# Optimization experiments

Measured on AMD Instinct MI355X. Metric: run time of the kernel, lower is better.

## Reference

```python
import jax, jax.numpy as jnp
import numpy as np
from functools import partial

BS, NQ, NC, NG = 16, 1000, 80, 200
EPS = 0.1
ITERS = 100
ALPHA, GAMMA = 0.25, 2.0
CC, CB, CG, CBG = 2.0, 5.0, 2.0, 1.0  # cost_class, cost_bbox, cost_giou, cost_bg
K, T_ITERS, T_CUR = 4, 6, 6


def setup_inputs() -> dict:
    key = jax.random.key(0)
    k0, k1, k2, k3 = jax.random.split(key, 4)
    pred_logits = jax.random.normal(k0, (BS, NQ, NC), jnp.float32)
    u = jax.random.uniform(k1, (BS, NQ, 4), jnp.float32)
    # valid xyxy boxes in image coordinates
    pred_boxes = jnp.concatenate([u[..., :2] * 1000.0,
                                  u[..., :2] * 1000.0 + u[..., 2:] * 200.0 + 1.0], axis=-1)
    gt_classes = jax.random.randint(k2, (BS, NG), 0, NC)
    v = jax.random.uniform(k3, (BS, NG, 4), jnp.float32)
    gt_boxes = jnp.concatenate([v[..., :2] * 1000.0,
                                v[..., :2] * 1000.0 + v[..., 2:] * 200.0 + 1.0], axis=-1)
    image_size_xyxy = jnp.tile(jnp.array([1333.0, 800.0, 1333.0, 800.0], jnp.float32), (BS, 1))
    image_size_xyxy_tgt = jnp.tile(image_size_xyxy[:, None, :], (1, NG, 1))
    return {"pred_logits": pred_logits, "pred_boxes": pred_boxes,
            "gt_classes": gt_classes, "gt_boxes": gt_boxes,
            "image_size_xyxy": image_size_xyxy, "image_size_xyxy_tgt": image_size_xyxy_tgt}


def pairwise_giou(a, b):
    # a: [G,4] xyxy, b: [Q,4] xyxy -> [G,Q]
    area_a = (a[:, 2] - a[:, 0]) * (a[:, 3] - a[:, 1])
    area_b = (b[:, 2] - b[:, 0]) * (b[:, 3] - b[:, 1])
    lt = jnp.maximum(a[:, None, :2], b[None, :, :2])
    rb = jnp.minimum(a[:, None, 2:], b[None, :, 2:])
    wh = jnp.clip(rb - lt, 0.0)
    inter = wh[..., 0] * wh[..., 1]
    union = area_a[:, None] + area_b[None, :] - inter
    iou = inter / union
    lt_c = jnp.minimum(a[:, None, :2], b[None, :, :2])
    rb_c = jnp.maximum(a[:, None, 2:], b[None, :, 2:])
    wh_c = jnp.clip(rb_c - lt_c, 0.0)
    area_c = wh_c[..., 0] * wh_c[..., 1]
    return iou - (area_c - union) / area_c


def sinkhorn_logdomain(mu, nu, C):
    # log-domain Sinkhorn, faithful to the torch loop (v update uses M^T)
    log_mu = jnp.log(mu + 1e-8)
    log_nu = jnp.log(nu + 1e-8)
    M = lambda u, v: (-C + u[:, None] + v[None, :]) / EPS

    def step(carry, _):
        u, v = carry
        v = EPS * (log_nu - jax.nn.logsumexp(M(u, v), axis=0)) + v
        u = EPS * (log_mu - jax.nn.logsumexp(M(u, v), axis=1)) + u
        return (u, v), None

    (u, v), _ = jax.lax.scan(step, (jnp.ones_like(mu), jnp.ones_like(nu)), None, length=ITERS)
    return jnp.exp(M(u, v))


def _per_image(logits, boxes, tgt_ids, tgt_bbox, img, img_tgt):
    # focal-loss classification cost without materializing [G,Q,C]:
    # for one-hot targets, loss_cls[g,q] = sum_c neg[q,c] + pos[q,id_g] - neg[q,id_g]
    p = jax.nn.sigmoid(logits)                                  # [Q,C]
    pos = ALPHA * jax.nn.softplus(-logits) * (1.0 - p) ** GAMMA  # target=1 term
    neg = (1.0 - ALPHA) * jax.nn.softplus(logits) * p ** GAMMA   # target=0 term
    neg_sum = neg.sum(axis=-1)                                   # [Q]
    delta = (pos - neg)[:, tgt_ids]                              # [Q,G]
    loss_cls = neg_sum[None, :] + delta.T                        # [G,Q]
    loss_bg = neg_sum                                            # [Q]

    out_b = boxes / img[None, :]
    tgt_b = tgt_bbox / img_tgt
    cost_bbox = jnp.abs(tgt_b[:, None, :] - out_b[None, :, :]).sum(-1)  # L1 cdist [G,Q]
    cost_giou = -pairwise_giou(tgt_bbox, boxes)                          # [G,Q]

    loss = CC * loss_cls + CB * cost_bbox + CG * cost_giou
    loss = jnp.concatenate([loss, CBG * loss_bg[None, :]], axis=0)       # [G+1,Q]

    # mu construction, faithful to original (scalar broadcast onto mu[:-1])
    fg = float(K) - 0.5 * (T_ITERS - T_CUR)
    mu_fg = float(NQ) - fg * NG
    mu = jnp.concatenate([jnp.full((NG,), mu_fg, loss.dtype), jnp.ones((1,), loss.dtype)])
    nu = jnp.ones((NQ,), loss.dtype)

    pi = sinkhorn_logdomain(mu, nu, loss)
    pi = pi / pi.max(axis=1, keepdims=True)
    matched_gt_inds = jnp.argmax(pi, axis=0)  # [Q], value NG means background
    return pi, matched_gt_inds


def reference(pred_logits, pred_boxes, gt_classes, gt_boxes, image_size_xyxy, image_size_xyxy_tgt):
    return jax.vmap(_per_image)(pred_logits, pred_boxes, gt_classes, gt_boxes,
                                image_size_xyxy, image_size_xyxy_tgt)
```

## Files before the change

kernel.cpp:

```cpp
#include <hip/hip_runtime.h>
#include <math.h>

#define NIMG 16
#define NQI  1000
#define NCC  80
#define NGG  200
#define RR   201
#define NR   208
#define RPT  13
#define NWG  16
#define CPW  63
#define NTHR 1024
#define NITER 100
#define LDW  68

#define LOG2E  1.4426950408889634f
#define SC     14.426950408889634f
#define U2INIT 14.426950408889634f
#define NEG    -1e30f

union MS { unsigned long long u; float2 f; };

__device__ __forceinline__ void img_barrier(unsigned* c, unsigned target) {
    __syncthreads();
    if (threadIdx.x == 0) {
        __hip_atomic_fetch_add(c, 1u, __ATOMIC_RELAXED, __HIP_MEMORY_SCOPE_AGENT);
        int spins = 0;
        while (__hip_atomic_load(c, __ATOMIC_RELAXED, __HIP_MEMORY_SCOPE_AGENT) < target) {
            if (++spins > (1 << 22)) break;
        }
    }
    __syncthreads();
}

extern "C" __global__ void __launch_bounds__(NTHR, 1)
ota_kernel(const float* __restrict__ logits,
           const float* __restrict__ pboxes,
           const int*   __restrict__ gcls,
           const float* __restrict__ gboxes,
           const float* __restrict__ imsz,
           const float* __restrict__ imszt,
           float* __restrict__ out,
           unsigned* __restrict__ cnt,
           unsigned long long* __restrict__ pms,
           float* __restrict__ pmx)
{
    const int tid = threadIdx.x;
    const int bid = blockIdx.x;
    const int img = (bid & 7) * 2 + ((bid >> 3) >> 4);
    const int wg  = (bid >> 3) & 15;
    const int q0  = wg * CPW;
    const int ncols = min(CPW, NQI - q0);
    unsigned* myc = cnt + img * 16;

    __shared__ __align__(16) float sA[NR * LDW];
    __shared__ float sU[NR];
    __shared__ float sRM[NR];

    float4* sTB4 = (float4*)sA;
    float4* sGB4 = (float4*)(sA + 800);
    float*  sGA  = sA + 1600;
    int*    sCL  = (int*)(sA + 1800);

    const float LMU2 = log2f(200.0f);

    for (int g = tid; g < NGG; g += NTHR) {
        float4 gb = *(const float4*)(gboxes + ((size_t)img * NGG + g) * 4);
        float4 t4 = *(const float4*)(imszt  + ((size_t)img * NGG + g) * 4);
        sGB4[g] = gb;
        sTB4[g] = make_float4(gb.x / t4.x, gb.y / t4.y, gb.z / t4.z, gb.w / t4.w);
        sGA[g] = (gb.z - gb.x) * (gb.w - gb.y);
        sCL[g] = gcls[(size_t)img * NGG + g];
    }
    if (tid < NR) sU[tid] = (tid < RR) ? U2INIT : NEG;
    __syncthreads();

    const int col  = tid >> 4;
    const int part = tid & 15;
    const int q    = q0 + col;
    const int r0   = part * RPT;

    const float* lp = logits + ((size_t)img * NQI + q) * NCC;

    float ns = 0.f;
    if (col < ncols) {
        for (int c = part; c < NCC; c += 16) {
            float l = lp[c];
            float p = 1.f / (1.f + exp2f(-l * LOG2E));
            float spl = fmaxf(l, 0.f) + log1pf(expf(-fabsf(l)));
            ns += 0.75f * spl * p * p;
        }
    }
    #pragma unroll
    for (int k = 1; k < 16; k <<= 1) ns += __shfl_xor(ns, k);

    float e[RPT];
    {
        float4 isz = *(const float4*)(imsz + img * 4);
        float4 pp = make_float4(0.f, 0.f, 0.f, 0.f);
        float ab = 0.f, ob0 = 0.f, ob1 = 0.f, ob2 = 0.f, ob3 = 0.f;
        if (col < ncols) {
            pp = *(const float4*)(pboxes + ((size_t)img * NQI + q) * 4);
            ab  = (pp.z - pp.x) * (pp.w - pp.y);
            ob0 = pp.x / isz.x; ob1 = pp.y / isz.y; ob2 = pp.z / isz.z; ob3 = pp.w / isz.w;
        }
        #pragma unroll
        for (int i = 0; i < RPT; ++i) {
            int g = r0 + i;
            float val = NEG;
            if (col < ncols) {
                if (g < NGG) {
                    float l = lp[sCL[g]];
                    float p = 1.f / (1.f + exp2f(-l * LOG2E));
                    float t0 = log1pf(expf(-fabsf(l)));
                    float spl  = fmaxf(l, 0.f) + t0;
                    float spml = spl - l;
                    float pos = 0.25f * spml * (1.f - p) * (1.f - p);
                    float neg = 0.75f * spl * p * p;
                    float lcls = ns + (pos - neg);
                    float4 tb = sTB4[g];
                    float cb = fabsf(tb.x - ob0) + fabsf(tb.y - ob1)
                             + fabsf(tb.z - ob2) + fabsf(tb.w - ob3);
                    float4 gb = sGB4[g];
                    float iwd = fminf(gb.z, pp.z) - fmaxf(gb.x, pp.x);
                    float ihd = fminf(gb.w, pp.w) - fmaxf(gb.y, pp.y);
                    float inter = fmaxf(iwd, 0.f) * fmaxf(ihd, 0.f);
                    float uni = sGA[g] + ab - inter;
                    float iou = inter / uni;
                    float cwd = fmaxf(gb.z, pp.z) - fminf(gb.x, pp.x);
                    float chd = fmaxf(gb.w, pp.w) - fminf(gb.y, pp.y);
                    float ac = fmaxf(cwd, 0.f) * fmaxf(chd, 0.f);
                    float giou = iou - (ac - uni) / ac;
                    float loss = 2.f * lcls + 5.f * cb - 2.f * giou;
                    val = -loss * SC;
                } else if (g == NGG) {
                    val = -ns * SC;
                }
            }
            e[i] = val;
        }
    }
    __syncthreads();

    const int r2 = tid >> 2, h = tid & 3;
    float vv = NEG;

    for (int it = 0; it < NITER; ++it) {
        {
            float M = NEG;
            float xr[RPT];
            #pragma unroll
            for (int i = 0; i < RPT; ++i) {
                float x = e[i] + sU[r0 + i];
                xr[i] = x; M = fmaxf(M, x);
            }
            #pragma unroll
            for (int k = 1; k < 16; k <<= 1) M = fmaxf(M, __shfl_xor(M, k));
            float S = 0.f;
            #pragma unroll
            for (int i = 0; i < RPT; ++i) S += exp2f(xr[i] - M);
            #pragma unroll
            for (int k = 1; k < 16; k <<= 1) S += __shfl_xor(S, k);
            vv = -(M + log2f(S));
            if (col >= ncols) vv = NEG;
        }
        #pragma unroll
        for (int i = 0; i < RPT; ++i) sA[(r0 + i) * LDW + col] = e[i] + vv;
        __syncthreads();
        unsigned long long* pb = pms + ((size_t)(it & 1) * NIMG + img) * (RR * NWG);
        if (r2 < RR) {
            const float4* base = (const float4*)(sA + r2 * LDW + h * 16);
            float4 t0 = base[0], t1 = base[1], t2 = base[2], t3 = base[3];
            float M2 = fmaxf(
                fmaxf(fmaxf(fmaxf(t0.x, t0.y), fmaxf(t0.z, t0.w)),
                      fmaxf(fmaxf(t1.x, t1.y), fmaxf(t1.z, t1.w))),
                fmaxf(fmaxf(fmaxf(t2.x, t2.y), fmaxf(t2.z, t2.w)),
                      fmaxf(fmaxf(t3.x, t3.y), fmaxf(t3.z, t3.w))));
            #pragma unroll
            for (int k = 1; k < 4; k <<= 1) M2 = fmaxf(M2, __shfl_xor(M2, k));
            float S2 = exp2f(t0.x - M2) + exp2f(t0.y - M2) + exp2f(t0.z - M2) + exp2f(t0.w - M2)
                     + exp2f(t1.x - M2) + exp2f(t1.y - M2) + exp2f(t1.z - M2) + exp2f(t1.w - M2)
                     + exp2f(t2.x - M2) + exp2f(t2.y - M2) + exp2f(t2.z - M2) + exp2f(t2.w - M2)
                     + exp2f(t3.x - M2) + exp2f(t3.y - M2) + exp2f(t3.z - M2) + exp2f(t3.w - M2);
            #pragma unroll
            for (int k = 1; k < 4; k <<= 1) S2 += __shfl_xor(S2, k);
            if (h == 0) {
                MS ms; ms.f.x = M2; ms.f.y = S2;
                __hip_atomic_store(&pb[r2 * NWG + wg], ms.u,
                                   __ATOMIC_RELAXED, __HIP_MEMORY_SCOPE_AGENT);
            }
        }
        img_barrier(myc, (unsigned)NWG * (it + 1));
        if (r2 < NR) {
            if (r2 < RR) {
                unsigned long long* pr = pb + r2 * NWG + h * 4;
                MS a0, a1, a2, a3;
                a0.u = __hip_atomic_load(&pr[0], __ATOMIC_RELAXED, __HIP_MEMORY_SCOPE_AGENT);
                a1.u = __hip_atomic_load(&pr[1], __ATOMIC_RELAXED, __HIP_MEMORY_SCOPE_AGENT);
                a2.u = __hip_atomic_load(&pr[2], __ATOMIC_RELAXED, __HIP_MEMORY_SCOPE_AGENT);
                a3.u = __hip_atomic_load(&pr[3], __ATOMIC_RELAXED, __HIP_MEMORY_SCOPE_AGENT);
                float gm = fmaxf(fmaxf(a0.f.x, a1.f.x), fmaxf(a2.f.x, a3.f.x));
                #pragma unroll
                for (int k = 1; k < 4; k <<= 1) gm = fmaxf(gm, __shfl_xor(gm, k));
                float S = a0.f.y * exp2f(a0.f.x - gm) + a1.f.y * exp2f(a1.f.x - gm)
                        + a2.f.y * exp2f(a2.f.x - gm) + a3.f.y * exp2f(a3.f.x - gm);
                #pragma unroll
                for (int k = 1; k < 4; k <<= 1) S += __shfl_xor(S, k);
                if (h == 0) sU[r2] = (r2 < NGG ? LMU2 : 0.f) - (gm + log2f(S));
            } else if (h == 0) {
                sU[r2] = NEG;
            }
        }
        __syncthreads();
    }

    float u2[RPT];
    #pragma unroll
    for (int i = 0; i < RPT; ++i) u2[i] = sU[r0 + i];
    #pragma unroll
    for (int i = 0; i < RPT; ++i) sA[(r0 + i) * LDW + col] = e[i] + u2[i] + vv;
    __syncthreads();
    if (r2 < RR) {
        const float4* base = (const float4*)(sA + r2 * LDW + h * 16);
        float4 t0 = base[0], t1 = base[1], t2 = base[2], t3 = base[3];
        float M2 = fmaxf(
            fmaxf(fmaxf(fmaxf(t0.x, t0.y), fmaxf(t0.z, t0.w)),
                  fmaxf(fmaxf(t1.x, t1.y), fmaxf(t1.z, t1.w))),
            fmaxf(fmaxf(fmaxf(t2.x, t2.y), fmaxf(t2.z, t2.w)),
                  fmaxf(fmaxf(t3.x, t3.y), fmaxf(t3.z, t3.w))));
        #pragma unroll
        for (int k = 1; k < 4; k <<= 1) M2 = fmaxf(M2, __shfl_xor(M2, k));
        if (h == 0)
            __hip_atomic_store(&pmx[((size_t)img * RR + r2) * NWG + wg], M2,
                               __ATOMIC_RELAXED, __HIP_MEMORY_SCOPE_AGENT);
    }
    img_barrier(myc, (unsigned)NWG * (NITER + 1));
    if (r2 < NR) {
        if (r2 < RR) {
            float* px = pmx + ((size_t)img * RR + r2) * NWG + h * 4;
            float M = fmaxf(
                fmaxf(__hip_atomic_load(&px[0], __ATOMIC_RELAXED, __HIP_MEMORY_SCOPE_AGENT),
                      __hip_atomic_load(&px[1], __ATOMIC_RELAXED, __HIP_MEMORY_SCOPE_AGENT)),
                fmaxf(__hip_atomic_load(&px[2], __ATOMIC_RELAXED, __HIP_MEMORY_SCOPE_AGENT),
                      __hip_atomic_load(&px[3], __ATOMIC_RELAXED, __HIP_MEMORY_SCOPE_AGENT)));
            #pragma unroll
            for (int k = 1; k < 4; k <<= 1) M = fmaxf(M, __shfl_xor(M, k));
            if (h == 0) sRM[r2] = M;
        } else if (h == 0) sRM[r2] = 0.f;
    }
    __syncthreads();

    {
        float bv = -3.0e38f; int bi = 0;
        #pragma unroll
        for (int i = 0; i < RPT; ++i) {
            int r = r0 + i;
            float key = e[i] + u2[i] - sRM[r];
            if (r < RR && key > bv) { bv = key; bi = r; }
        }
        #pragma unroll
        for (int k = 1; k < 16; k <<= 1) {
            float ov = __shfl_xor(bv, k); int oi = __shfl_xor(bi, k);
            if (ov > bv || (ov == bv && oi < bi)) { bv = ov; bi = oi; }
        }
        if (part == 0 && col < ncols)
            out[(size_t)NIMG * RR * NQI + (size_t)img * NQI + q] = (float)bi;
    }

    for (int c = 0; c < 4; ++c) {
        __syncthreads();
        if ((part >> 2) == c && col < ncols) {
            #pragma unroll
            for (int i = 0; i < RPT; ++i) {
                int r = r0 + i;
                if (r < RR)
                    sA[(r - 52 * c) * LDW + col] = exp2f(e[i] + u2[i] + vv - sRM[r]);
            }
        }
        __syncthreads();
        int rl = tid >> 6, colj = tid & 63;
        #pragma unroll
        for (int t = 0; t < 4; ++t) {
            int rr = rl + 16 * t, rg = 52 * c + rr;
            if (rr < 52 && rg < RR && colj < ncols)
                out[((size_t)img * RR + rg) * NQI + (q0 + colj)] = sA[rr * LDW + colj];
        }
    }
}

extern "C" void kernel_launch(void* const* d_in, const int* in_sizes, int n_in,
                              void* d_out, int out_size, void* d_ws, size_t ws_size,
                              hipStream_t stream) {
    const float* logits = (const float*)d_in[0];
    const float* pboxes = (const float*)d_in[1];
    const int*   gcls   = (const int*)  d_in[2];
    const float* gboxes = (const float*)d_in[3];
    const float* imsz   = (const float*)d_in[4];
    const float* imszt  = (const float*)d_in[5];
    float* out = (float*)d_out;

    unsigned* cnt = (unsigned*)d_ws;
    unsigned long long* pms = (unsigned long long*)((char*)d_ws + 1024);
    float* pmx = (float*)((char*)d_ws + 1024 + 2ull * NIMG * RR * NWG * 8);

    hipMemsetAsync(d_ws, 0, 1024, stream);

    ota_kernel<<<dim3(256), dim3(NTHR), 0, stream>>>(
        logits, pboxes, gcls, gboxes, imsz, imszt, out, cnt, pms, pmx);
}
```

Before: 534.9 us.

## Replace per-iteration image barrier with tagged per-row flags and linear-domain Sinkhorn

Moves Sinkhorn iterations 2..100 from log-sum-exp with max tracking to a linear-domain form: column normalisation produces scaled probabilities whose row sums are exchanged as plain floats. The global atomic counter barrier is replaced by per-slot tagged values (sum plus iteration tag), so each row waits only on its own 16 partials instead of a workgroup-wide barrier. The final output writes are also collapsed into a single pass. This cuts exp/max work and barrier latency, at the cost of possible underflow in the linear domain and reliance on tag polling over a larger memset workspace.

```diff
diff --git a/kernel.cpp b/kernel.cpp
--- a/kernel.cpp
+++ b/kernel.cpp
@@ -42,8 +42,8 @@
            const float* __restrict__ imszt,
            float* __restrict__ out,
            unsigned* __restrict__ cnt,
-           unsigned long long* __restrict__ pms,
-           float* __restrict__ pmx)
+           unsigned long long* __restrict__ pmsB,
+           unsigned long long* __restrict__ pmsA)
 {
     const int tid = threadIdx.x;
     const int bid = blockIdx.x;
@@ -72,7 +72,6 @@
         sGA[g] = (gb.z - gb.x) * (gb.w - gb.y);
         sCL[g] = gcls[(size_t)img * NGG + g];
     }
-    if (tid < NR) sU[tid] = (tid < RR) ? U2INIT : NEG;
     __syncthreads();
 
     const int col  = tid >> 4;
@@ -143,31 +142,126 @@
     __syncthreads();
 
     const int r2 = tid >> 2, h = tid & 3;
-    float vv = NEG;
-
-    for (int it = 0; it < NITER; ++it) {
-        {
-            float M = NEG;
-            float xr[RPT];
+    const int r2c = min(r2, RR - 1);
+
+    float vv;
+    {
+        float M = NEG; float xr[RPT];
+        #pragma unroll
+        for (int i = 0; i < RPT; ++i) { xr[i] = e[i] + U2INIT; M = fmaxf(M, xr[i]); }
+        #pragma unroll
+        for (int k = 1; k < 16; k <<= 1) M = fmaxf(M, __shfl_xor(M, k));
+        float S = 0.f;
+        #pragma unroll
+        for (int i = 0; i < RPT; ++i) S += exp2f(xr[i] - M);
+        #pragma unroll
+        for (int k = 1; k < 16; k <<= 1) S += __shfl_xor(S, k);
+        vv = -(M + log2f(S));
+        if (col >= ncols) vv = NEG;
+    }
+    #pragma unroll
+    for (int i = 0; i < RPT; ++i) sA[(r0 + i) * LDW + col] = e[i] + vv;
+    __syncthreads();
+    if (r2 < RR) {
+        const float4* base = (const float4*)(sA + r2 * LDW + h * 16);
+        float4 t0 = base[0], t1 = base[1], t2 = base[2], t3 = base[3];
+        float M2 = fmaxf(
+            fmaxf(fmaxf(fmaxf(t0.x, t0.y), fmaxf(t0.z, t0.w)),
+                  fmaxf(fmaxf(t1.x, t1.y), fmaxf(t1.z, t1.w))),
+            fmaxf(fmaxf(fmaxf(t2.x, t2.y), fmaxf(t2.z, t2.w)),
+                  fmaxf(fmaxf(t3.x, t3.y), fmaxf(t3.z, t3.w))));
+        #pragma unroll
+        for (int k = 1; k < 4; k <<= 1) M2 = fmaxf(M2, __shfl_xor(M2, k));
+        float S2 = exp2f(t0.x - M2) + exp2f(t0.y - M2) + exp2f(t0.z - M2) + exp2f(t0.w - M2)
+                 + exp2f(t1.x - M2) + exp2f(t1.y - M2) + exp2f(t1.z - M2) + exp2f(t1.w - M2)
+                 + exp2f(t2.x - M2) + exp2f(t2.y - M2) + exp2f(t2.z - M2) + exp2f(t2.w - M2)
+                 + exp2f(t3.x - M2) + exp2f(t3.y - M2) + exp2f(t3.z - M2) + exp2f(t3.w - M2);
+        #pragma unroll
+        for (int k = 1; k < 4; k <<= 1) S2 += __shfl_xor(S2, k);
+        if (h == 0) {
+            MS ms; ms.f.x = M2; ms.f.y = S2;
+            __hip_atomic_store(&pmsA[((size_t)img * RR + r2) * NWG + wg], ms.u,
+                               __ATOMIC_RELAXED, __HIP_MEMORY_SCOPE_AGENT);
+        }
+    }
+    img_barrier(myc, NWG);
+    if (r2 < NR) {
+        if (r2 < RR) {
+            unsigned long long* pr = pmsA + ((size_t)img * RR + r2) * NWG + h * 4;
+            MS a0, a1, a2, a3;
+            a0.u = __hip_atomic_load(&pr[0], __ATOMIC_RELAXED, __HIP_MEMORY_SCOPE_AGENT);
+            a1.u = __hip_atomic_load(&pr[1], __ATOMIC_RELAXED, __HIP_MEMORY_SCOPE_AGENT);
+            a2.u = __hip_atomic_load(&pr[2], __ATOMIC_RELAXED, __HIP_MEMORY_SCOPE_AGENT);
+            a3.u = __hip_atomic_load(&pr[3], __ATOMIC_RELAXED, __HIP_MEMORY_SCOPE_AGENT);
+            float gm = fmaxf(fmaxf(a0.f.x, a1.f.x), fmaxf(a2.f.x, a3.f.x));
             #pragma unroll
-            for (int i = 0; i < RPT; ++i) {
-                float x = e[i] + sU[r0 + i];
-                xr[i] = x; M = fmaxf(M, x);
-            }
+            for (int k = 1; k < 4; k <<= 1) gm = fmaxf(gm, __shfl_xor(gm, k));
+            float S = a0.f.y * exp2f(a0.f.x - gm) + a1.f.y * exp2f(a1.f.x - gm)
+                    + a2.f.y * exp2f(a2.f.x - gm) + a3.f.y * exp2f(a3.f.x - gm);
             #pragma unroll
-            for (int k = 1; k < 16; k <<= 1) M = fmaxf(M, __shfl_xor(M, k));
-            float S = 0.f;
-            #pragma unroll
-            for (int i = 0; i < RPT; ++i) S += exp2f(xr[i] - M);
-            #pragma unroll
-            for (int k = 1; k < 16; k <<= 1) S += __shfl_xor(S, k);
-            vv = -(M + log2f(S));
-            if (col >= ncols) vv = NEG;
-        }
-        #pragma unroll
-        for (int i = 0; i < RPT; ++i) sA[(r0 + i) * LDW + col] = e[i] + vv;
+            for (int k = 1; k < 4; k <<= 1) S += __shfl_xor(S, k);
+            if (h == 0) sU[r2] = (r2 < NGG ? LMU2 : 0.f) - (gm + log2f(S));
+        } else if (h == 0) sU[r2] = NEG;
+    }
+    __syncthreads();
+
+    for (int it = 2; it <= NITER; ++it) {
+        const float tagf = (float)it;
+        float t[RPT]; float cs = 0.f;
+        #pragma unroll
+        for (int i = 0; i < RPT; ++i) {
+            t[i] = exp2f(e[i] + sU[r0 + i] + vv);
+            cs += t[i];
+        }
+        #pragma unroll
+        for (int k = 1; k < 16; k <<= 1) cs += __shfl_xor(cs, k);
+        float cf = 0.f;
+        if (col < ncols) { vv -= log2f(cs); cf = 1.0f / cs; }
+        #pragma unroll
+        for (int i = 0; i < RPT; ++i) sA[(r0 + i) * LDW + col] = t[i] * cf;
         __syncthreads();
-        unsigned long long* pb = pms + ((size_t)(it & 1) * NIMG + img) * (RR * NWG);
+        unsigned long long* slot =
+            pmsB + (((size_t)(it & 1) * NIMG + img) * RR + r2c) * NWG;
+        if (r2 < RR) {
+            const float4* base = (const float4*)(sA + r2 * LDW + h * 16);
+            float4 t0 = base[0], t1 = base[1], t2 = base[2], t3 = base[3];
+            float s = (t0.x + t0.y + t0.z + t0.w) + (t1.x + t1.y + t1.z + t1.w)
+                    + (t2.x + t2.y + t2.z + t2.w) + (t3.x + t3.y + t3.z + t3.w);
+            s += __shfl_xor(s, 1); s += __shfl_xor(s, 2);
+            if (h == 0) {
+                MS ms; ms.f.x = s; ms.f.y = tagf;
+                __hip_atomic_store(&slot[wg], ms.u,
+                                   __ATOMIC_RELAXED, __HIP_MEMORY_SCOPE_AGENT);
+            }
+            unsigned long long* pr = slot + 4 * h;
+            MS a0, a1, a2, a3;
+            int spins = 0;
+            for (;;) {
+                a0.u = __hip_atomic_load(&pr[0], __ATOMIC_RELAXED, __HIP_MEMORY_SCOPE_AGENT);
+                a1.u = __hip_atomic_load(&pr[1], __ATOMIC_RELAXED, __HIP_MEMORY_SCOPE_AGENT);
+                a2.u = __hip_atomic_load(&pr[2], __ATOMIC_RELAXED, __HIP_MEMORY_SCOPE_AGENT);
+                a3.u = __hip_atomic_load(&pr[3], __ATOMIC_RELAXED, __HIP_MEMORY_SCOPE_AGENT);
+                if ((a0.f.y == tagf) && (a1.f.y == tagf) &&
+                    (a2.f.y == tagf) && (a3.f.y == tagf)) break;
+                if (++spins > (1 << 22)) break;
+            }
+            float R = (a0.f.x + a1.f.x) + (a2.f.x + a3.f.x);
+            R += __shfl_xor(R, 1); R += __shfl_xor(R, 2);
+            if (h == 0) sU[r2] += (r2 < NGG ? LMU2 : 0.f) - log2f(R);
+        }
+        __syncthreads();
+    }
+
+    float p[RPT];
+    #pragma unroll
+    for (int i = 0; i < RPT; ++i) p[i] = exp2f(e[i] + sU[r0 + i] + vv);
+    #pragma unroll
+    for (int i = 0; i < RPT; ++i) sA[(r0 + i) * LDW + col] = p[i];
+    __syncthreads();
+    {
+        const float tagf = (float)(NITER + 1);
+        unsigned long long* slot =
+            pmsB + (((size_t)((NITER + 1) & 1) * NIMG + img) * RR + r2c) * NWG;
         if (r2 < RR) {
             const float4* base = (const float4*)(sA + r2 * LDW + h * 16);
             float4 t0 = base[0], t1 = base[1], t2 = base[2], t3 = base[3];
@@ -178,85 +272,38 @@
                       fmaxf(fmaxf(t3.x, t3.y), fmaxf(t3.z, t3.w))));
             #pragma unroll
             for (int k = 1; k < 4; k <<= 1) M2 = fmaxf(M2, __shfl_xor(M2, k));
-            float S2 = exp2f(t0.x - M2) + exp2f(t0.y - M2) + exp2f(t0.z - M2) + exp2f(t0.w - M2)
-                     + exp2f(t1.x - M2) + exp2f(t1.y - M2) + exp2f(t1.z - M2) + exp2f(t1.w - M2)
-                     + exp2f(t2.x - M2) + exp2f(t2.y - M2) + exp2f(t2.z - M2) + exp2f(t2.w - M2)
-                     + exp2f(t3.x - M2) + exp2f(t3.y - M2) + exp2f(t3.z - M2) + exp2f(t3.w - M2);
-            #pragma unroll
-            for (int k = 1; k < 4; k <<= 1) S2 += __shfl_xor(S2, k);
             if (h == 0) {
-                MS ms; ms.f.x = M2; ms.f.y = S2;
-                __hip_atomic_store(&pb[r2 * NWG + wg], ms.u,
+                MS ms; ms.f.x = M2; ms.f.y = tagf;
+                __hip_atomic_store(&slot[wg], ms.u,
                                    __ATOMIC_RELAXED, __HIP_MEMORY_SCOPE_AGENT);
             }
-        }
-        img_barrier(myc, (unsigned)NWG * (it + 1));
-        if (r2 < NR) {
-            if (r2 < RR) {
-                unsigned long long* pr = pb + r2 * NWG + h * 4;
-                MS a0, a1, a2, a3;
+            unsigned long long* pr = slot + 4 * h;
+            MS a0, a1, a2, a3;
+            int spins = 0;
+            for (;;) {
                 a0.u = __hip_atomic_load(&pr[0], __ATOMIC_RELAXED, __HIP_MEMORY_SCOPE_AGENT);
                 a1.u = __hip_atomic_load(&pr[1], __ATOMIC_RELAXED, __HIP_MEMORY_SCOPE_AGENT);
                 a2.u = __hip_atomic_load(&pr[2], __ATOMIC_RELAXED, __HIP_MEMORY_SCOPE_AGENT);
                 a3.u = __hip_atomic_load(&pr[3], __ATOMIC_RELAXED, __HIP_MEMORY_SCOPE_AGENT);
-                float gm = fmaxf(fmaxf(a0.f.x, a1.f.x), fmaxf(a2.f.x, a3.f.x));
-                #pragma unroll
-                for (int k = 1; k < 4; k <<= 1) gm = fmaxf(gm, __shfl_xor(gm, k));
-                float S = a0.f.y * exp2f(a0.f.x - gm) + a1.f.y * exp2f(a1.f.x - gm)
-                        + a2.f.y * exp2f(a2.f.x - gm) + a3.f.y * exp2f(a3.f.x - gm);
-                #pragma unroll
-                for (int k = 1; k < 4; k <<= 1) S += __shfl_xor(S, k);
-                if (h == 0) sU[r2] = (r2 < NGG ? LMU2 : 0.f) - (gm + log2f(S));
-            } else if (h == 0) {
-                sU[r2] = NEG;
-            }
-        }
-        __syncthreads();
-    }
-
-    float u2[RPT];
-    #pragma unroll
-    for (int i = 0; i < RPT; ++i) u2[i] = sU[r0 + i];
-    #pragma unroll
-    for (int i = 0; i < RPT; ++i) sA[(r0 + i) * LDW + col] = e[i] + u2[i] + vv;
-    __syncthreads();
-    if (r2 < RR) {
-        const float4* base = (const float4*)(sA + r2 * LDW + h * 16);
-        float4 t0 = base[0], t1 = base[1], t2 = base[2], t3 = base[3];
-        float M2 = fmaxf(
-            fmaxf(fmaxf(fmaxf(t0.x, t0.y), fmaxf(t0.z, t0.w)),
-                  fmaxf(fmaxf(t1.x, t1.y), fmaxf(t1.z, t1.w))),
-            fmaxf(fmaxf(fmaxf(t2.x, t2.y), fmaxf(t2.z, t2.w)),
-                  fmaxf(fmaxf(t3.x, t3.y), fmaxf(t3.z, t3.w))));
-        #pragma unroll
-        for (int k = 1; k < 4; k <<= 1) M2 = fmaxf(M2, __shfl_xor(M2, k));
-        if (h == 0)
-            __hip_atomic_store(&pmx[((size_t)img * RR + r2) * NWG + wg], M2,
-                               __ATOMIC_RELAXED, __HIP_MEMORY_SCOPE_AGENT);
-    }
-    img_barrier(myc, (unsigned)NWG * (NITER + 1));
-    if (r2 < NR) {
-        if (r2 < RR) {
-            float* px = pmx + ((size_t)img * RR + r2) * NWG + h * 4;
-            float M = fmaxf(
-                fmaxf(__hip_atomic_load(&px[0], __ATOMIC_RELAXED, __HIP_MEMORY_SCOPE_AGENT),
-                      __hip_atomic_load(&px[1], __ATOMIC_RELAXED, __HIP_MEMORY_SCOPE_AGENT)),
-                fmaxf(__hip_atomic_load(&px[2], __ATOMIC_RELAXED, __HIP_MEMORY_SCOPE_AGENT),
-                      __hip_atomic_load(&px[3], __ATOMIC_RELAXED, __HIP_MEMORY_SCOPE_AGENT)));
+                if ((a0.f.y == tagf) && (a1.f.y == tagf) &&
+                    (a2.f.y == tagf) && (a3.f.y == tagf)) break;
+                if (++spins > (1 << 22)) break;
+            }
+            float M = fmaxf(fmaxf(a0.f.x, a1.f.x), fmaxf(a2.f.x, a3.f.x));
             #pragma unroll
             for (int k = 1; k < 4; k <<= 1) M = fmaxf(M, __shfl_xor(M, k));
             if (h == 0) sRM[r2] = M;
-        } else if (h == 0) sRM[r2] = 0.f;
-    }
-    __syncthreads();
-
-    {
-        float bv = -3.0e38f; int bi = 0;
+        } else if (r2 < NR && h == 0) sRM[r2] = 1.0f;
+        __syncthreads();
+    }
+
+    {
+        float bv = -1.0f; int bi = 0x7fffffff;
         #pragma unroll
         for (int i = 0; i < RPT; ++i) {
             int r = r0 + i;
-            float key = e[i] + u2[i] - sRM[r];
-            if (r < RR && key > bv) { bv = key; bi = r; }
+            float pv = p[i] / sRM[r];
+            if (r < RR && pv > bv) { bv = pv; bi = r; }
         }
         #pragma unroll
         for (int k = 1; k < 16; k <<= 1) {
@@ -267,23 +314,14 @@
             out[(size_t)NIMG * RR * NQI + (size_t)img * NQI + q] = (float)bi;
     }
 
-    for (int c = 0; c < 4; ++c) {
-        __syncthreads();
-        if ((part >> 2) == c && col < ncols) {
-            #pragma unroll
-            for (int i = 0; i < RPT; ++i) {
-                int r = r0 + i;
-                if (r < RR)
-                    sA[(r - 52 * c) * LDW + col] = exp2f(e[i] + u2[i] + vv - sRM[r]);
-            }
-        }
-        __syncthreads();
-        int rl = tid >> 6, colj = tid & 63;
-        #pragma unroll
-        for (int t = 0; t < 4; ++t) {
-            int rr = rl + 16 * t, rg = 52 * c + rr;
-            if (rr < 52 && rg < RR && colj < ncols)
-                out[((size_t)img * RR + rg) * NQI + (q0 + colj)] = sA[rr * LDW + colj];
+    {
+        int colj = tid & 63, rl = tid >> 6;
+        #pragma unroll
+        for (int tt = 0; tt < RPT; ++tt) {
+            int rg = rl + 16 * tt;
+            if (rg < RR && colj < ncols)
+                out[((size_t)img * RR + rg) * NQI + (q0 + colj)] =
+                    sA[rg * LDW + colj] / sRM[rg];
         }
     }
 }
@@ -300,11 +338,12 @@
     float* out = (float*)d_out;
 
     unsigned* cnt = (unsigned*)d_ws;
-    unsigned long long* pms = (unsigned long long*)((char*)d_ws + 1024);
-    float* pmx = (float*)((char*)d_ws + 1024 + 2ull * NIMG * RR * NWG * 8);
-
-    hipMemsetAsync(d_ws, 0, 1024, stream);
+    unsigned long long* pmsB = (unsigned long long*)((char*)d_ws + 1024);
+    unsigned long long* pmsA =
+        (unsigned long long*)((char*)d_ws + 1024 + 2ull * NIMG * RR * NWG * 8);
+
+    hipMemsetAsync(d_ws, 0, 1024 + 2ull * NIMG * RR * NWG * 8, stream);
 
     ota_kernel<<<dim3(256), dim3(NTHR), 0, stream>>>(
-        logits, pboxes, gcls, gboxes, imsz, imszt, out, cnt, pms, pmx);
+        logits, pboxes, gcls, gboxes, imsz, imszt, out, cnt, pmsB, pmsA);
 }
```

Measured after the change: 1.758 ms. 3.29x slower.
